# Performance work log

Hardware: AMD Instinct MI355X
Metric: run time of the kernel (lower is better)

Reference implementation:

```python
import jax, jax.numpy as jnp
import numpy as np

B, L, D = 2, 2048, 1024
NUM_HEADS = 16
HEAD_DIM = D // NUM_HEADS


def setup_inputs() -> dict:
    key = jax.random.key(0)
    k1, k2 = jax.random.split(key)
    x = jax.random.normal(k1, (B, L, D), dtype=jnp.float32)
    # torch Linear(input_dim, 3*output_dim, bias=False); store as [in, 3*out] for x @ W
    W_qkv = jax.random.normal(k2, (D, 3 * D), dtype=jnp.float32) * (1.0 / np.sqrt(D))
    return {"x": x, "W_qkv": W_qkv}


def reference(x, W_qkv):
    b, l, d = x.shape
    h, hd = NUM_HEADS, HEAD_DIM
    qkv = x @ W_qkv                                  # [B, L, 3*D]
    qkv = qkv.reshape(b, l, 3, h, hd)
    q = jnp.transpose(qkv[:, :, 0], (0, 2, 1, 3))    # [B, H, L, hd]
    k = jnp.transpose(qkv[:, :, 1], (0, 2, 1, 3))
    v = jnp.transpose(qkv[:, :, 2], (0, 2, 1, 3))
    scale = 1.0 / jnp.sqrt(jnp.asarray(hd, dtype=x.dtype))
    scores = jnp.einsum('bhqd,bhkd->bhqk', q, k) * scale   # [B, H, L, L]
    causal = jnp.triu(jnp.ones((l, l), dtype=bool), k=1)   # True above diagonal -> masked
    scores = jnp.where(causal, -jnp.inf, scores)
    attn = jax.nn.softmax(scores, axis=-1)
    # dropout p=0.0 -> identity (eval mode)
    out = jnp.einsum('bhqk,bhkd->bhqd', attn, v)            # [B, H, L, hd]
    out = jnp.transpose(out, (0, 2, 1, 3)).reshape(b, l, h * hd)
    return out
```

## Files before the change

kernel.cpp:

```cpp
#include <hip/hip_runtime.h>
#include <hip/hip_bf16.h>
#include <math.h>

#define NB_L 2048
#define GM 4096
#define GN 3072
#define GK 1024
#define NROWS 65536
#define SCALE_L2E 0.180336880f

typedef float  f4v __attribute__((ext_vector_type(4)));
typedef short  s4v __attribute__((ext_vector_type(4)));
typedef short  s8v __attribute__((ext_vector_type(8)));

#define MFMA_16x16x32(a, b, c) __builtin_amdgcn_mfma_f32_16x16x32_bf16((a), (b), (c), 0, 0, 0)
#define MFMA_16x16x16(a, b, c) __builtin_amdgcn_mfma_f32_16x16x16bf16_1k((a), (b), (c), 0, 0, 0)

static __device__ __forceinline__ unsigned int bfpk(float a, float b) {
    __hip_bfloat162 h = __float22bfloat162_rn(float2{a, b});
    union { __hip_bfloat162 h2; unsigned int u; } cv; cv.h2 = h; return cv.u;
}
static __device__ __forceinline__ unsigned short bf1(float a) {
    union { __hip_bfloat16 h; unsigned short u; } cv; cv.h = __float2bfloat16(a); return cv.u;
}
static __device__ __forceinline__ float bf2f(unsigned short u) {
    union { unsigned int u; float f; } cv; cv.u = ((unsigned int)u) << 16; return cv.f;
}

static __device__ __forceinline__ void gl_lds16(const ushort* g, ushort* l) {
    __builtin_amdgcn_global_load_lds((const __attribute__((address_space(1))) void*)g,
                                     (__attribute__((address_space(3))) void*)l, 16, 0, 0);
}

__global__ __launch_bounds__(256) void conv_fused(
    const float* __restrict__ X, const float* __restrict__ W,
    ushort* __restrict__ Xb, ushort* __restrict__ Wt)
{
    __shared__ __align__(16) ushort T[64][72];
    const int bid = blockIdx.x, t = threadIdx.x;
    if (bid < 2048) {
        const int i = bid * 256 + t;
        const float4 f0 = ((const float4*)X)[2 * i];
        const float4 f1 = ((const float4*)X)[2 * i + 1];
        uint4 u;
        u.x = bfpk(f0.x, f0.y); u.y = bfpk(f0.z, f0.w);
        u.z = bfpk(f1.x, f1.y); u.w = bfpk(f1.z, f1.w);
        ((uint4*)Xb)[i] = u;
    } else {
        const int wb = bid - 2048;
        const int k0 = (wb & 15) * 64, n0 = (wb >> 4) * 64;
        {
            const int kr = t >> 2, nc0 = (t & 3) * 16;
            const float* src = W + (size_t)(k0 + kr) * GN + n0 + nc0;
#pragma unroll
            for (int u = 0; u < 4; ++u) {
                const float4 v = *(const float4*)(src + 4 * u);
                T[nc0 + 4 * u + 0][kr] = bf1(v.x);
                T[nc0 + 4 * u + 1][kr] = bf1(v.y);
                T[nc0 + 4 * u + 2][kr] = bf1(v.z);
                T[nc0 + 4 * u + 3][kr] = bf1(v.w);
            }
        }
        __syncthreads();
        {
            const int nr = t >> 2, kc0 = (t & 3) * 16;
            ushort* dst = Wt + (size_t)(n0 + nr) * GK + k0 + kc0;
            *(s8v*)dst       = *(const s8v*)&T[nr][kc0];
            *(s8v*)(dst + 8) = *(const s8v*)&T[nr][kc0 + 8];
        }
    }
}

__global__ __launch_bounds__(256) void qkv_gemm_bf16(
    const ushort* __restrict__ Xb, const ushort* __restrict__ Wt,
    ushort* __restrict__ Qh, ushort* __restrict__ Kh, ushort* __restrict__ VT)
{
    __shared__ __align__(16) ushort As[2][4][128][8];
    __shared__ __align__(16) ushort Bs[2][4][128][8];
    const int tid = threadIdx.x;

    const int l = blockIdx.x;
    const int j = l & 7, t = l >> 3;
    const int lr = t & 7, lc = t >> 3;
    const int ytile = ((j >> 1) << 3) + lr;
    const int xtile = (j & 1) * 12 + lc;
    const int row0 = ytile * 128, col0 = xtile * 128;

    const int mA = tid & 127, k2a = tid >> 7;
    const int lane = tid & 63, w = tid >> 6;
    const int wr = w >> 1, wc = w & 1, lq = lane & 15, quad = lane >> 4;

    f4v acc[4][4];
#pragma unroll
    for (int g = 0; g < 4; ++g)
#pragma unroll
        for (int j2 = 0; j2 < 4; ++j2) acc[g][j2] = 0.f;

    const ushort* gA = Xb + (size_t)(row0 + mA) * GK + k2a * 8;
    const ushort* gB = Wt + (size_t)(col0 + mA) * GK + k2a * 8;

    gl_lds16(gA,      &As[0][k2a][mA][0]);
    gl_lds16(gA + 16, &As[0][k2a + 2][mA][0]);
    gl_lds16(gB,      &Bs[0][k2a][mA][0]);
    gl_lds16(gB + 16, &Bs[0][k2a + 2][mA][0]);

    for (int it = 0; it < 32; ++it) {
        const int cur = it & 1, nxt = cur ^ 1;
        __syncthreads();
        if (it + 1 < 32) {
            const int k0 = (it + 1) * 32;
            gl_lds16(gA + k0,      &As[nxt][k2a][mA][0]);
            gl_lds16(gA + k0 + 16, &As[nxt][k2a + 2][mA][0]);
            gl_lds16(gB + k0,      &Bs[nxt][k2a][mA][0]);
            gl_lds16(gB + k0 + 16, &Bs[nxt][k2a + 2][mA][0]);
        }
        s8v af[4], bfr[4];
#pragma unroll
        for (int g = 0; g < 4; ++g) af[g]   = *(const s8v*)&As[cur][quad][wr * 64 + g * 16 + lq][0];
#pragma unroll
        for (int j2 = 0; j2 < 4; ++j2) bfr[j2] = *(const s8v*)&Bs[cur][quad][wc * 64 + j2 * 16 + lq][0];
#pragma unroll
        for (int g = 0; g < 4; ++g)
#pragma unroll
            for (int j2 = 0; j2 < 4; ++j2)
                acc[g][j2] = MFMA_16x16x32(af[g], bfr[j2], acc[g][j2]);
    }

    const int part = xtile >> 3;
#pragma unroll
    for (int g = 0; g < 4; ++g)
#pragma unroll
        for (int j2 = 0; j2 < 4; ++j2) {
            const int colp = (col0 & 1023) + wc * 64 + j2 * 16 + lq;
            const int hh = colp >> 6, d = colp & 63;
#pragma unroll
            for (int r = 0; r < 4; ++r) {
                const int row = row0 + wr * 64 + g * 16 + quad * 4 + r;
                const int b = row >> 11, tok = row & 2047;
                const int bh = b * 16 + hh;
                if (part == 0) {
                    Qh[((size_t)bh * 2048 + tok) * 64 + d] = bf1(acc[g][j2][r] * SCALE_L2E);
                } else if (part == 1) {
                    Kh[((size_t)bh * 2048 + tok) * 64 + (d ^ ((tok & 7) << 3))] = bf1(acc[g][j2][r]);
                } else {
                    VT[((size_t)bh * 64 + d) * 2048 + (tok ^ ((d & 7) << 3))] = bf1(acc[g][j2][r]);
                }
            }
        }
}

__global__ __launch_bounds__(256, 4) void attn_bf16(
    const ushort* __restrict__ Qh, const ushort* __restrict__ Kh,
    const ushort* __restrict__ VT, ushort* __restrict__ Opart, float* __restrict__ Lp)
{
    __shared__ __align__(16) ushort Ks[2][64 * 64];
    __shared__ __align__(16) ushort Vt[2][64 * 64];

    const int x = blockIdx.x;
    const int bh = x & 31;
    const int qlow = (x >> 5) & 7;
    const int s = (x >> 8) & 1;
    const int x9 = (x >> 9) & 1;
    const int qt = x9 ? (15 - qlow) : qlow;

    const int tid = threadIdx.x;
    const int w = tid >> 6, lane = tid & 63;
    const int lq = lane & 15, quad = lane >> 4;
    const int kswz = (lq & 7) << 3;
    const int qrow_base = qt * 128 + w * 32;
    const int diag = 2 * qt + (w >> 1);

    s8v qf[2][2];
#pragma unroll
    for (int qg = 0; qg < 2; ++qg)
#pragma unroll
        for (int sb = 0; sb < 2; ++sb)
            qf[qg][sb] = *(const s8v*)(Qh + ((size_t)bh * 2048 + qrow_base + qg * 16 + lq) * 64
                                       + sb * 32 + quad * 8);

    f4v o[4][2];
#pragma unroll
    for (int dg = 0; dg < 4; ++dg)
#pragma unroll
        for (int qg = 0; qg < 2; ++qg) o[dg][qg] = 0.f;
    f4v lacc[2]; lacc[0] = 0.f; lacc[1] = 0.f;
    const s4v ones = { (short)0x3F80, (short)0x3F80, (short)0x3F80, (short)0x3F80 };

    const int kt_lo = s ? (qt + 1) : 0;
    const int kt_hi = s ? (2 * qt + 1) : qt;
    const int niter = kt_hi - kt_lo + 1;

    const ushort* kbase = Kh + (size_t)bh * 2048 * 64;
    const ushort* vbase = VT + (size_t)bh * 64 * 2048;
    const int g1 = tid, g2 = tid + 256;
    const int kr1 = g1 >> 3, ko1 = (g1 & 7) * 8;
    const int kr2 = g2 >> 3, ko2 = (g2 & 7) * 8;

    auto stage = [&](int kt, int bufi) {
        const ushort* kt_k = kbase + (size_t)kt * 64 * 64;
        const ushort* kt_v = vbase + kt * 64;
        gl_lds16(kt_k + kr1 * 64 + ko1,           &Ks[bufi][g1 * 8]);
        gl_lds16(kt_k + kr2 * 64 + ko2,           &Ks[bufi][g2 * 8]);
        gl_lds16(kt_v + (size_t)kr1 * 2048 + ko1, &Vt[bufi][g1 * 8]);
        gl_lds16(kt_v + (size_t)kr2 * 2048 + ko2, &Vt[bufi][g2 * 8]);
    };

    auto compute = [&](int ktc, int bufi) {
        if (ktc > diag) return;
        f4v st[4][2];
#pragma unroll
        for (int kg = 0; kg < 4; ++kg)
#pragma unroll
            for (int qg = 0; qg < 2; ++qg) st[kg][qg] = 0.f;
#pragma unroll
        for (int kg = 0; kg < 4; ++kg)
#pragma unroll
            for (int sb = 0; sb < 2; ++sb) {
                const s8v af = *(const s8v*)&Ks[bufi][(kg * 16 + lq) * 64
                                                     + ((sb * 32 + quad * 8) ^ kswz)];
#pragma unroll
                for (int qg = 0; qg < 2; ++qg)
                    st[kg][qg] = MFMA_16x16x32(af, qf[qg][sb], st[kg][qg]);
            }
        if (ktc == diag) {
#pragma unroll
            for (int kg = 0; kg < 4; ++kg)
#pragma unroll
                for (int qg = 0; qg < 2; ++qg) {
                    const int qrow = qrow_base + qg * 16 + lq;
#pragma unroll
                    for (int r = 0; r < 4; ++r)
                        if (ktc * 64 + kg * 16 + quad * 4 + r > qrow)
                            st[kg][qg][r] = -INFINITY;
                }
        }
#pragma unroll
        for (int kg = 0; kg < 4; ++kg)
#pragma unroll
            for (int qg = 0; qg < 2; ++qg)
#pragma unroll
                for (int r = 0; r < 4; ++r)
                    st[kg][qg][r] = exp2f(st[kg][qg][r]);
#pragma unroll
        for (int ks = 0; ks < 4; ++ks) {
            s4v pb[2];
#pragma unroll
            for (int qg = 0; qg < 2; ++qg) {
                union { s4v v; uint2 u; } c;
                c.u.x = bfpk(st[ks][qg][0], st[ks][qg][1]);
                c.u.y = bfpk(st[ks][qg][2], st[ks][qg][3]);
                pb[qg] = c.v;
            }
#pragma unroll
            for (int qg = 0; qg < 2; ++qg)
                lacc[qg] = MFMA_16x16x16(ones, pb[qg], lacc[qg]);
#pragma unroll
            for (int dg = 0; dg < 4; ++dg) {
                const s4v va = *(const s4v*)&Vt[bufi][(dg * 16 + lq) * 64
                                                     + ((ks * 16 + quad * 4) ^ kswz)];
#pragma unroll
                for (int qg = 0; qg < 2; ++qg)
                    o[dg][qg] = MFMA_16x16x16(va, pb[qg], o[dg][qg]);
            }
        }
    };

    stage(kt_lo, 0);
    for (int i = 0; i < niter; ++i) {
        const int cur = i & 1;
        __syncthreads();
        if (i + 1 < niter) stage(kt_lo + i + 1, cur ^ 1);
        compute(kt_lo + i, cur);
    }

#pragma unroll
    for (int qg = 0; qg < 2; ++qg) {
        const size_t prow = (size_t)(s * 32 + bh) * 2048 + qrow_base + qg * 16 + lq;
#pragma unroll
        for (int dg = 0; dg < 4; ++dg) {
            const int d = dg * 16 + quad * 4;
            uint2 u;
            u.x = bfpk(o[dg][qg][0], o[dg][qg][1]);
            u.y = bfpk(o[dg][qg][2], o[dg][qg][3]);
            *(uint2*)&Opart[prow * 64 + d] = u;
        }
        if (quad == 0) Lp[prow] = lacc[qg][0];
    }
}

__global__ __launch_bounds__(256) void attn_combine(
    const ushort* __restrict__ Opart, const float* __restrict__ Lp, float* __restrict__ Out)
{
    const int id = blockIdx.x * 256 + threadIdx.x;
    const int row = id >> 4, c4 = (id & 15) * 4;
    const float l0 = Lp[row], l1 = Lp[row + NROWS];
    const float inv = 1.0f / (l0 + l1);

    const s4v a = *(const s4v*)&Opart[(size_t)row * 64 + c4];
    const s4v c = *(const s4v*)&Opart[(size_t)(row + NROWS) * 64 + c4];
    float4 v;
    v.x = (bf2f((unsigned short)a[0]) + bf2f((unsigned short)c[0])) * inv;
    v.y = (bf2f((unsigned short)a[1]) + bf2f((unsigned short)c[1])) * inv;
    v.z = (bf2f((unsigned short)a[2]) + bf2f((unsigned short)c[2])) * inv;
    v.w = (bf2f((unsigned short)a[3]) + bf2f((unsigned short)c[3])) * inv;

    const int bh = row >> 11, qrow = row & 2047;
    const int b = bh >> 4, h = bh & 15;
    *(float4*)(Out + ((size_t)(b * 2048 + qrow)) * 1024 + h * 64 + c4) = v;
}

extern "C" void kernel_launch(void* const* d_in, const int* in_sizes, int n_in,
                              void* d_out, int out_size, void* d_ws, size_t ws_size,
                              hipStream_t stream)
{
    const float* x  = (const float*)d_in[0];
    const float* wq = (const float*)d_in[1];
    float* out = (float*)d_out;

    const size_t HEADTEN = (size_t)32 * 2048 * 64;
    ushort* wsp = (ushort*)d_ws;
    ushort* qh = wsp;
    ushort* kh = qh + HEADTEN;
    ushort* vt = kh + HEADTEN;
    ushort* xb = vt + HEADTEN;
    ushort* wt = xb + (size_t)GM * GK;
    ushort* opart = xb;
    float*  lp    = (float*)(opart + (size_t)2 * NROWS * 64);

    conv_fused<<<2816, 256, 0, stream>>>(x, wq, xb, wt);
    qkv_gemm_bf16<<<768, 256, 0, stream>>>(xb, wt, qh, kh, vt);
    attn_bf16<<<1024, 256, 0, stream>>>(qh, kh, vt, opart, lp);
    attn_combine<<<NROWS * 16 / 256, 256, 0, stream>>>(opart, lp, out);
}
```

Measured before the change: 190.3 us.

## Rework QKV GEMM into 256x256 tiles with 512 threads and staged pipelining

```diff
diff --git a/kernel.cpp b/kernel.cpp
--- a/kernel.cpp
+++ b/kernel.cpp
@@ -71,79 +71,147 @@
     }
 }
 
-__global__ __launch_bounds__(256) void qkv_gemm_bf16(
+__global__ __launch_bounds__(512, 2) void qkv_gemm_bf16(
     const ushort* __restrict__ Xb, const ushort* __restrict__ Wt,
     ushort* __restrict__ Qh, ushort* __restrict__ Kh, ushort* __restrict__ VT)
 {
-    __shared__ __align__(16) ushort As[2][4][128][8];
-    __shared__ __align__(16) ushort Bs[2][4][128][8];
+    __shared__ __align__(16) ushort As[2][2][256][32];
+    __shared__ __align__(16) ushort Bs[2][2][256][32];
+
     const int tid = threadIdx.x;
-
-    const int l = blockIdx.x;
-    const int j = l & 7, t = l >> 3;
-    const int lr = t & 7, lc = t >> 3;
-    const int ytile = ((j >> 1) << 3) + lr;
-    const int xtile = (j & 1) * 12 + lc;
-    const int row0 = ytile * 128, col0 = xtile * 128;
-
-    const int mA = tid & 127, k2a = tid >> 7;
+    const int bid = blockIdx.x;
+
+    const int xcd = bid & 7, idx = bid >> 3;
+    const int ytile = ((xcd >> 1) << 2) + (idx & 3);
+    const int xtile = (xcd & 1) * 6 + (idx >> 2);
+    const int row0 = ytile << 8, col0 = xtile << 8;
+
     const int lane = tid & 63, w = tid >> 6;
-    const int wr = w >> 1, wc = w & 1, lq = lane & 15, quad = lane >> 4;
-
-    f4v acc[4][4];
-#pragma unroll
-    for (int g = 0; g < 4; ++g)
-#pragma unroll
-        for (int j2 = 0; j2 < 4; ++j2) acc[g][j2] = 0.f;
-
-    const ushort* gA = Xb + (size_t)(row0 + mA) * GK + k2a * 8;
-    const ushort* gB = Wt + (size_t)(col0 + mA) * GK + k2a * 8;
-
-    gl_lds16(gA,      &As[0][k2a][mA][0]);
-    gl_lds16(gA + 16, &As[0][k2a + 2][mA][0]);
-    gl_lds16(gB,      &Bs[0][k2a][mA][0]);
-    gl_lds16(gB + 16, &Bs[0][k2a + 2][mA][0]);
-
-    for (int it = 0; it < 32; ++it) {
-        const int cur = it & 1, nxt = cur ^ 1;
-        __syncthreads();
-        if (it + 1 < 32) {
-            const int k0 = (it + 1) * 32;
-            gl_lds16(gA + k0,      &As[nxt][k2a][mA][0]);
-            gl_lds16(gA + k0 + 16, &As[nxt][k2a + 2][mA][0]);
-            gl_lds16(gB + k0,      &Bs[nxt][k2a][mA][0]);
-            gl_lds16(gB + k0 + 16, &Bs[nxt][k2a + 2][mA][0]);
-        }
+    const int wm = w >> 2, wn = w & 3;
+    const int lq = lane & 15, quad = lane >> 4;
+
+    const int rA = tid >> 2, pA = tid & 3;
+    const int cA = pA ^ ((rA >> 1) & 3);
+    const ushort* gA0 = Xb + (size_t)(row0 + rA) * GK + cA * 8;
+    const ushort* gB0 = Wt + (size_t)(col0 + rA) * GK + cA * 8;
+
+    const int pq = (quad ^ ((lq >> 1) & 3)) * 8;
+    const int rowA = wm * 128 + lq;
+    const int rowB = wn * 64 + lq;
+
+    f4v acc[8][4];
+#pragma unroll
+    for (int mf = 0; mf < 8; ++mf)
+#pragma unroll
+        for (int nf = 0; nf < 4; ++nf) acc[mf][nf] = 0.f;
+
+    auto stA = [&](int t, int h, int u) {
+        gl_lds16(gA0 + (size_t)u * 128 * GK + t * 64 + h * 32,
+                 &As[t & 1][h][u * 128 + rA][pA * 8]);
+    };
+    auto stB = [&](int t, int h, int u) {
+        gl_lds16(gB0 + (size_t)u * 128 * GK + t * 64 + h * 32,
+                 &Bs[t & 1][h][u * 128 + rA][pA * 8]);
+    };
+
+    stA(0, 0, 0); stA(0, 0, 1);
+    stB(0, 0, 0); stB(0, 0, 1);
+    stB(0, 1, 0); stB(0, 1, 1);
+    stA(0, 1, 0); stA(0, 1, 1);
+    stA(1, 0, 0); stA(1, 0, 1);
+    stB(1, 0, 0); stB(1, 0, 1);
+    asm volatile("s_waitcnt vmcnt(4)" ::: "memory");
+    __builtin_amdgcn_s_barrier();
+    asm volatile("" ::: "memory");
+
+    const int NT = GK / 64;
+#pragma unroll 2
+    for (int t = 0; t < NT; ++t) {
+        const int cur = t & 1;
         s8v af[4], bfr[4];
-#pragma unroll
-        for (int g = 0; g < 4; ++g) af[g]   = *(const s8v*)&As[cur][quad][wr * 64 + g * 16 + lq][0];
-#pragma unroll
-        for (int j2 = 0; j2 < 4; ++j2) bfr[j2] = *(const s8v*)&Bs[cur][quad][wc * 64 + j2 * 16 + lq][0];
-#pragma unroll
-        for (int g = 0; g < 4; ++g)
-#pragma unroll
-            for (int j2 = 0; j2 < 4; ++j2)
-                acc[g][j2] = MFMA_16x16x32(af[g], bfr[j2], acc[g][j2]);
+
+#pragma unroll
+        for (int nf = 0; nf < 4; ++nf) bfr[nf] = *(const s8v*)&Bs[cur][0][rowB + nf * 16][pq];
+#pragma unroll
+        for (int mf = 0; mf < 4; ++mf) af[mf] = *(const s8v*)&As[cur][0][rowA + mf * 16][pq];
+        if (t + 1 < NT) { stB(t + 1, 1, 0); stB(t + 1, 1, 1); }
+        __builtin_amdgcn_s_barrier();
+        asm volatile("s_waitcnt lgkmcnt(0)");
+        __builtin_amdgcn_s_setprio(1);
+#pragma unroll
+        for (int mf = 0; mf < 4; ++mf)
+#pragma unroll
+            for (int nf = 0; nf < 4; ++nf)
+                acc[mf][nf] = MFMA_16x16x32(af[mf], bfr[nf], acc[mf][nf]);
+        __builtin_amdgcn_s_setprio(0);
+        __builtin_amdgcn_s_barrier();
+
+#pragma unroll
+        for (int mf = 0; mf < 4; ++mf) af[mf] = *(const s8v*)&As[cur][0][rowA + 64 + mf * 16][pq];
+        if (t + 1 < NT) { stA(t + 1, 1, 0); stA(t + 1, 1, 1); }
+        __builtin_amdgcn_s_barrier();
+        asm volatile("s_waitcnt lgkmcnt(0)");
+        __builtin_amdgcn_s_setprio(1);
+#pragma unroll
+        for (int mf = 0; mf < 4; ++mf)
+#pragma unroll
+            for (int nf = 0; nf < 4; ++nf)
+                acc[mf + 4][nf] = MFMA_16x16x32(af[mf], bfr[nf], acc[mf + 4][nf]);
+        __builtin_amdgcn_s_setprio(0);
+        __builtin_amdgcn_s_barrier();
+
+#pragma unroll
+        for (int nf = 0; nf < 4; ++nf) bfr[nf] = *(const s8v*)&Bs[cur][1][rowB + nf * 16][pq];
+#pragma unroll
+        for (int mf = 0; mf < 4; ++mf) af[mf] = *(const s8v*)&As[cur][1][rowA + mf * 16][pq];
+        if (t + 2 < NT) { stA(t + 2, 0, 0); stA(t + 2, 0, 1); }
+        __builtin_amdgcn_s_barrier();
+        asm volatile("s_waitcnt lgkmcnt(0)");
+        __builtin_amdgcn_s_setprio(1);
+#pragma unroll
+        for (int mf = 0; mf < 4; ++mf)
+#pragma unroll
+            for (int nf = 0; nf < 4; ++nf)
+                acc[mf][nf] = MFMA_16x16x32(af[mf], bfr[nf], acc[mf][nf]);
+        __builtin_amdgcn_s_setprio(0);
+        __builtin_amdgcn_s_barrier();
+
+#pragma unroll
+        for (int mf = 0; mf < 4; ++mf) af[mf] = *(const s8v*)&As[cur][1][rowA + 64 + mf * 16][pq];
+        if (t + 2 < NT) { stB(t + 2, 0, 0); stB(t + 2, 0, 1); }
+        __builtin_amdgcn_s_barrier();
+        asm volatile("s_waitcnt lgkmcnt(0)");
+        __builtin_amdgcn_s_setprio(1);
+#pragma unroll
+        for (int mf = 0; mf < 4; ++mf)
+#pragma unroll
+            for (int nf = 0; nf < 4; ++nf)
+                acc[mf + 4][nf] = MFMA_16x16x32(af[mf], bfr[nf], acc[mf + 4][nf]);
+        __builtin_amdgcn_s_setprio(0);
+        if (t + 2 < NT) asm volatile("s_waitcnt vmcnt(4)" ::: "memory");
+        else            asm volatile("s_waitcnt vmcnt(0)" ::: "memory");
+        __builtin_amdgcn_s_barrier();
+        asm volatile("" ::: "memory");
     }
 
-    const int part = xtile >> 3;
-#pragma unroll
-    for (int g = 0; g < 4; ++g)
-#pragma unroll
-        for (int j2 = 0; j2 < 4; ++j2) {
-            const int colp = (col0 & 1023) + wc * 64 + j2 * 16 + lq;
+    const int part = xtile >> 2;
+#pragma unroll
+    for (int mf = 0; mf < 8; ++mf)
+#pragma unroll
+        for (int nf = 0; nf < 4; ++nf) {
+            const int colp = (col0 & 1023) + wn * 64 + nf * 16 + lq;
             const int hh = colp >> 6, d = colp & 63;
 #pragma unroll
             for (int r = 0; r < 4; ++r) {
-                const int row = row0 + wr * 64 + g * 16 + quad * 4 + r;
+                const int row = row0 + wm * 128 + mf * 16 + quad * 4 + r;
                 const int b = row >> 11, tok = row & 2047;
                 const int bh = b * 16 + hh;
                 if (part == 0) {
-                    Qh[((size_t)bh * 2048 + tok) * 64 + d] = bf1(acc[g][j2][r] * SCALE_L2E);
+                    Qh[((size_t)bh * 2048 + tok) * 64 + d] = bf1(acc[mf][nf][r] * SCALE_L2E);
                 } else if (part == 1) {
-                    Kh[((size_t)bh * 2048 + tok) * 64 + (d ^ ((tok & 7) << 3))] = bf1(acc[g][j2][r]);
+                    Kh[((size_t)bh * 2048 + tok) * 64 + (d ^ ((tok & 7) << 3))] = bf1(acc[mf][nf][r]);
                 } else {
-                    VT[((size_t)bh * 64 + d) * 2048 + (tok ^ ((d & 7) << 3))] = bf1(acc[g][j2][r]);
+                    VT[((size_t)bh * 64 + d) * 2048 + (tok ^ ((d & 7) << 3))] = bf1(acc[mf][nf][r]);
                 }
             }
         }
@@ -328,7 +396,7 @@
     float*  lp    = (float*)(opart + (size_t)2 * NROWS * 64);
 
     conv_fused<<<2816, 256, 0, stream>>>(x, wq, xb, wt);
-    qkv_gemm_bf16<<<768, 256, 0, stream>>>(xb, wt, qh, kh, vt);
+    qkv_gemm_bf16<<<192, 512, 0, stream>>>(xb, wt, qh, kh, vt);
     attn_bf16<<<1024, 256, 0, stream>>>(qh, kh, vt, opart, lp);
     attn_combine<<<NROWS * 16 / 256, 256, 0, stream>>>(opart, lp, out);
 }
```

New measurement: 177.6 us. 6.6% less time.
